# Optimization experiments

Hardware: AMD Instinct MI355X
Metric: run time of the kernel (lower is better)

Reference implementation:

```python
import jax, jax.numpy as jnp
import numpy as np

EMBED_DIM = 768
NUM_HEADS = 8
HEAD_DIM = EMBED_DIM // NUM_HEADS  # 96
SCALE = HEAD_DIM ** -0.5


def setup_inputs() -> dict:
    key = jax.random.key(0)
    k1, k2, k3 = jax.random.split(key, 3)
    x = jax.random.normal(k1, (2, 4096, EMBED_DIM), dtype=jnp.float32)
    # nn.Linear weights stored [out, in]; init scaled like kaiming-uniform-ish
    w_qkv = jax.random.normal(k2, (3 * EMBED_DIM, EMBED_DIM), dtype=jnp.float32) * (EMBED_DIM ** -0.5)
    w_proj = jax.random.normal(k3, (EMBED_DIM, EMBED_DIM), dtype=jnp.float32) * (EMBED_DIM ** -0.5)
    return {"x": x, "w_qkv": w_qkv, "w_proj": w_proj}


def reference(x, w_qkv, w_proj):
    B, N, C = x.shape
    H, D = NUM_HEADS, C // NUM_HEADS
    qkv = jnp.einsum('bnc,oc->bno', x, w_qkv)          # [B,N,3C]
    qkv = qkv.reshape(B, N, 3, H, D).transpose(2, 0, 3, 1, 4)  # [3,B,H,N,D]
    q, k, v = qkv[0], qkv[1], qkv[2]
    attn = jnp.einsum('bhnd,bhmd->bhnm', q, k) * SCALE  # [B,H,N,N]
    attn = jax.nn.softmax(attn, axis=-1)
    out = jnp.einsum('bhnm,bhmd->bhnd', attn, v)        # [B,H,N,D]
    out = out.transpose(0, 2, 1, 3).reshape(B, N, C)
    out = jnp.einsum('bnc,oc->bno', out, w_proj)        # proj (no bias)
    return out  # dropout p=0.0 -> identity
```

## Files before the change

### kernel.cpp

```cpp
#include <hip/hip_runtime.h>

typedef __bf16 bf16;
typedef __attribute__((ext_vector_type(8))) __bf16 bf16x8;
typedef __attribute__((ext_vector_type(2))) __bf16 bf16x2;
typedef __attribute__((ext_vector_type(4))) float f32x4;
typedef __attribute__((ext_vector_type(16))) float f32x16;
typedef __attribute__((ext_vector_type(8))) unsigned short ushort8;
typedef __attribute__((ext_vector_type(4))) unsigned short ushort4v;

__device__ __forceinline__ unsigned short f2bf(float f) {
    union { float f; unsigned int u; } v; v.f = f;
    unsigned int u = v.u;
    return (unsigned short)((u + 0x7fffu + ((u >> 16) & 1u)) >> 16);
}

#if __has_builtin(__builtin_amdgcn_cvt_pk_bf16_f32)
__device__ __forceinline__ unsigned int pk2bf(float a, float b) {
    union { bf16x2 v; unsigned int u; } c;
    c.v = __builtin_amdgcn_cvt_pk_bf16_f32(a, b);
    return c.u;
}
#else
__device__ __forceinline__ unsigned int pk2bf(float a, float b) {
    return (unsigned int)f2bf(a) | ((unsigned int)f2bf(b) << 16);
}
#endif

__device__ __forceinline__ f32x4 mfma16(bf16x8 a, bf16x8 b, f32x4 c) {
    return __builtin_amdgcn_mfma_f32_16x16x32_bf16(a, b, c, 0, 0, 0);
}
__device__ __forceinline__ f32x16 mfma32(bf16x8 a, bf16x8 b, f32x16 c) {
    return __builtin_amdgcn_mfma_f32_32x32x16_bf16(a, b, c, 0, 0, 0);
}

#if __has_builtin(__builtin_amdgcn_global_load_lds)
__device__ __forceinline__ void gload16(const unsigned short* g, unsigned short* l) {
    typedef const unsigned int __attribute__((address_space(1)))* gp_t;
    typedef unsigned int __attribute__((address_space(3)))* lp_t;
    __builtin_amdgcn_global_load_lds((gp_t)(const void*)g, (lp_t)(void*)l, 16, 0, 0);
}
#define GLL_LANE 1
#else
#define GLL_LANE 0
#endif

__global__ void cvt3_f32_bf16(const float* __restrict__ x, const float* __restrict__ wq,
                              const float* __restrict__ wp,
                              unsigned short* __restrict__ xb, unsigned short* __restrict__ wqb,
                              unsigned short* __restrict__ wpb) {
    int i = blockIdx.x * 256 + threadIdx.x;
    const float* in; unsigned short* out; int base;
    if (i < 1572864)      { in = x;  out = xb;  base = i; }
    else if (i < 2015232) { in = wq; out = wqb; base = i - 1572864; }
    else if (i < 2162688) { in = wp; out = wpb; base = i - 2015232; }
    else return;
    float4 f = reinterpret_cast<const float4*>(in)[base];
    union { ushort4v v; unsigned int u[2]; } o;
    o.u[0] = pk2bf(f.x, f.y);
    o.u[1] = pk2bf(f.z, f.w);
    reinterpret_cast<ushort4v*>(out)[base] = o.v;
}

__device__ __forceinline__ int kperm(int k5) {
    return (k5 & 3) | (((k5 >> 3) & 1) << 2) | (((k5 >> 4) & 1) << 3) | (((k5 >> 2) & 1) << 4);
}
__device__ __forceinline__ int kperm_inv(int p5) {
    return (p5 & 3) | (((p5 >> 4) & 1) << 2) | (((p5 >> 2) & 1) << 3) | (((p5 >> 3) & 1) << 4);
}

__global__ __launch_bounds__(256) void qkv_gemm(const unsigned short* __restrict__ A,
                                                const unsigned short* __restrict__ W,
                                                unsigned short* __restrict__ Qf,
                                                unsigned short* __restrict__ Kf,
                                                unsigned short* __restrict__ Vf) {
    __shared__ __align__(16) char smem[34816];
    unsigned short* S = (unsigned short*)smem;
    unsigned short* T = (unsigned short*)smem;
    const int t = threadIdx.x;
    const int w = t >> 6, l = t & 63;
    const int wm = (w >> 1) * 64, wn = (w & 1) * 64;
    const int lr = l & 15, lq = l >> 4;
    const int lqs8 = (lq ^ ((lr >> 1) & 3)) * 8;
    const int m0 = blockIdx.y * 128, n0 = blockIdx.x * 128;
    f32x4 acc[4][4] = {};

#if GLL_LANE
#define QSTAGE(ks, boff)                                                        \
    {                                                                           \
        const int k0s = (ks) * 32;                                              \
        _Pragma("unroll")                                                       \
        for (int i = 0; i < 2; ++i) {                                           \
            int v = t + i * 256;                                                \
            int r = v >> 2, q8 = (((v & 3) ^ ((v >> 3) & 3)) * 8);              \
            unsigned short* dst = &S[(boff) + (w * 64 + i * 256) * 8];          \
            gload16(&A[(m0 + r) * 768 + k0s + q8], dst);                        \
            gload16(&W[(n0 + r) * 768 + k0s + q8], dst + 4096);                 \
        }                                                                       \
    }
#else
#define QSTAGE(ks, boff)                                                        \
    {                                                                           \
        const int k0s = (ks) * 32;                                              \
        _Pragma("unroll")                                                       \
        for (int i = 0; i < 2; ++i) {                                           \
            int v = t + i * 256;                                                \
            int r = v >> 2, q8 = (((v & 3) ^ ((v >> 3) & 3)) * 8);              \
            *reinterpret_cast<ushort8*>(&S[(boff) + v * 8]) =                   \
                *reinterpret_cast<const ushort8*>(&A[(m0 + r) * 768 + k0s + q8]);\
            *reinterpret_cast<ushort8*>(&S[(boff) + 4096 + v * 8]) =            \
                *reinterpret_cast<const ushort8*>(&W[(n0 + r) * 768 + k0s + q8]);\
        }                                                                       \
    }
#endif

    QSTAGE(0, 0);
    __syncthreads();
    for (int ks = 0; ks < 24; ++ks) {
        const int cur = (ks & 1) ? 8192 : 0;
        if (ks < 23) QSTAGE(ks + 1, 8192 - cur);
        bf16x8 af[4], bfr[4];
#pragma unroll
        for (int mt = 0; mt < 4; ++mt)
            af[mt] = *reinterpret_cast<const bf16x8*>(&S[cur + (wm + mt * 16 + lr) * 32 + lqs8]);
#pragma unroll
        for (int nt = 0; nt < 4; ++nt)
            bfr[nt] = *reinterpret_cast<const bf16x8*>(&S[cur + 4096 + (wn + nt * 16 + lr) * 32 + lqs8]);
#pragma unroll
        for (int mt = 0; mt < 4; ++mt)
#pragma unroll
            for (int nt = 0; nt < 4; ++nt)
                acc[mt][nt] = mfma16(af[mt], bfr[nt], acc[mt][nt]);
        __syncthreads();
    }
#undef QSTAGE
    const int tsel = n0 / 768;
    if (tsel < 2) {
#pragma unroll
        for (int nt = 0; nt < 4; ++nt)
#pragma unroll
            for (int mt = 0; mt < 4; ++mt)
#pragma unroll
                for (int r = 0; r < 4; ++r) {
                    int row = wm + mt * 16 + lq * 4 + r;
                    int col = wn + nt * 16 + lr;
                    float val = acc[mt][nt][r];
                    if (tsel == 0) val *= 0.14724444f;
                    T[row * 136 + col] = f2bf(val);
                }
    } else {
#pragma unroll
        for (int nt = 0; nt < 4; ++nt)
#pragma unroll
            for (int mt = 0; mt < 4; ++mt)
#pragma unroll
                for (int r = 0; r < 4; ++r) {
                    int row = wm + mt * 16 + lq * 4 + r;
                    int col = wn + nt * 16 + lr;
                    T[col * 136 + row] = f2bf(acc[mt][nt][r]);
                }
    }
    __syncthreads();
    if (tsel < 2) {
#pragma unroll
        for (int i = 0; i < 8; ++i) {
            int idx = t + i * 256;
            int pos31 = idx & 31;
            int rest = idx >> 5;
            int c8 = rest & 15, qg = rest >> 4;
            int l31 = (tsel == 1) ? kperm_inv(pos31) : pos31;
            int gncol = n0 + c8 * 8;
            int rem = gncol - tsel * 768;
            int head = rem / 96, d = rem - head * 96;
            int kq = d >> 4, h2 = (d >> 3) & 1;
            int gm = m0 + qg * 32 + l31;
            int b = gm >> 12, nn = gm & 4095;
            int bh = b * 8 + head;
            long chunk = (long)(bh * 128 + (nn >> 5)) * 6 + kq;
            ushort8 v8 = *reinterpret_cast<const ushort8*>(&T[(qg * 32 + l31) * 136 + c8 * 8]);
            unsigned short* dst = (tsel == 0) ? Qf : Kf;
            *reinterpret_cast<ushort8*>(&dst[(chunk << 9) + ((h2 * 32 + pos31) << 3)]) = v8;
        }
    } else {
#pragma unroll
        for (int i = 0; i < 8; ++i) {
            int idx = t + i * 256;
            int dl = idx & 31;
            int rr = idx >> 5;
            int r8 = rr & 15, cmb = rr >> 4;
            int col = cmb * 32 + dl;
            int gncol = n0 + col;
            int rem = gncol - 1536;
            int head = rem / 96, d = rem - head * 96;
            int dn = d >> 5;
            int keybase = m0 + r8 * 8;
            int b = keybase >> 12, nn = keybase & 4095;
            int kg = nn >> 5, f = (nn >> 4) & 1, hv = (nn >> 3) & 1;
            int bh = b * 8 + head;
            long chunk = (long)(bh * 128 + kg) * 6 + dn * 2 + f;
            ushort8 v8 = *reinterpret_cast<const ushort8*>(&T[col * 136 + r8 * 8]);
            *reinterpret_cast<ushort8*>(&Vf[(chunk << 9) + ((hv * 32 + dl) << 3)]) = v8;
        }
    }
}

__global__ __launch_bounds__(256, 2) void attn_kernel(const unsigned short* __restrict__ Qf,
                                                      const unsigned short* __restrict__ Kf,
                                                      const unsigned short* __restrict__ Vf,
                                                      unsigned short* __restrict__ Og) {
    __shared__ __align__(16) float red[4608];
    const int t = threadIdx.x;
    const int w = t >> 6, l = t & 63;
    const int wr = w >> 1, wk = w & 1;
    const int l31 = l & 31, h = l >> 5;
    const int b0 = blockIdx.x;
    const int kk = b0 >> 3;
    const int bh = (b0 & 7) * 2 + (kk >> 5);
    const int q0 = (kk & 31) * 128;
    const int voff = l << 3;

    bf16x8 aq[2][6];
#pragma unroll
    for (int qn = 0; qn < 2; ++qn) {
        long qb = ((long)((bh * 128 + (q0 >> 5) + wr * 2 + qn) * 6)) << 9;
#pragma unroll
        for (int kq = 0; kq < 6; ++kq)
            aq[qn][kq] = *reinterpret_cast<const bf16x8*>(&Qf[qb + (kq << 9) + voff]);
    }

    f32x16 acc[2][3] = {};
    float lsum0 = 0.f, lsum1 = 0.f;

    for (int it = 0; it < 64; ++it) {
        const int kt = wk * 64 + it;
        const long kbase = ((long)((bh * 128 + kt) * 6)) << 9;
        f32x16 s[2] = {};
#pragma unroll
        for (int kq = 0; kq < 6; ++kq) {
            bf16x8 bk = *reinterpret_cast<const bf16x8*>(&Kf[kbase + (kq << 9) + voff]);
            s[0] = mfma32(bk, aq[0][kq], s[0]);
            s[1] = mfma32(bk, aq[1][kq], s[1]);
        }
        union PF { unsigned int u[4]; bf16x8 v8; } p[2][2];
#pragma unroll
        for (int qn = 0; qn < 2; ++qn) {
            float e[16];
#pragma unroll
            for (int r = 0; r < 16; ++r) e[r] = __builtin_amdgcn_exp2f(s[qn][r]);
            float s0 = (e[0] + e[1]) + (e[2] + e[3]);
            float s1 = (e[4] + e[5]) + (e[6] + e[7]);
            float s2 = (e[8] + e[9]) + (e[10] + e[11]);
            float s3 = (e[12] + e[13]) + (e[14] + e[15]);
            if (qn == 0) lsum0 += (s0 + s1) + (s2 + s3);
            else         lsum1 += (s0 + s1) + (s2 + s3);
#pragma unroll
            for (int f = 0; f < 2; ++f) {
                p[qn][f].u[0] = pk2bf(e[4 * f + 0], e[4 * f + 1]);
                p[qn][f].u[1] = pk2bf(e[4 * f + 2], e[4 * f + 3]);
                p[qn][f].u[2] = pk2bf(e[8 + 4 * f + 0], e[8 + 4 * f + 1]);
                p[qn][f].u[3] = pk2bf(e[8 + 4 * f + 2], e[8 + 4 * f + 3]);
            }
        }
#pragma unroll
        for (int dn = 0; dn < 3; ++dn) {
#pragma unroll
            for (int f = 0; f < 2; ++f) {
                bf16x8 vb = *reinterpret_cast<const bf16x8*>(
                    &Vf[kbase + ((dn * 2 + f) << 9) + voff]);
                acc[0][dn] = mfma32(p[0][f].v8, vb, acc[0][dn]);
                acc[1][dn] = mfma32(p[1][f].v8, vb, acc[1][dn]);
            }
        }
    }

    const int rbase = (wr * 64 + l) * 36;
#pragma unroll
    for (int ps = 0; ps < 3; ++ps) {
        __syncthreads();
        if (wk == 1) {
#pragma unroll
            for (int c = 0; c < 2; ++c) {
                int c2 = ps * 2 + c, qn = c2 / 3, dn = c2 % 3;
#pragma unroll
                for (int u = 0; u < 4; ++u) {
                    f32x4 tmp;
#pragma unroll
                    for (int j = 0; j < 4; ++j) tmp[j] = acc[qn][dn][u * 4 + j];
                    *reinterpret_cast<f32x4*>(&red[rbase + c * 16 + u * 4]) = tmp;
                }
            }
        }
        __syncthreads();
        if (wk == 0) {
#pragma unroll
            for (int c = 0; c < 2; ++c) {
                int c2 = ps * 2 + c, qn = c2 / 3, dn = c2 % 3;
#pragma unroll
                for (int u = 0; u < 4; ++u) {
                    f32x4 tmp = *reinterpret_cast<const f32x4*>(&red[rbase + c * 16 + u * 4]);
#pragma unroll
                    for (int j = 0; j < 4; ++j) acc[qn][dn][u * 4 + j] += tmp[j];
                }
            }
        }
    }

    lsum0 += __shfl_xor(lsum0, 32);
    lsum1 += __shfl_xor(lsum1, 32);
    __syncthreads();
    if (wk == 1 && h == 0) {
        red[(wr * 2 + 0) * 32 + l31] = lsum0;
        red[(wr * 2 + 1) * 32 + l31] = lsum1;
    }
    __syncthreads();
    if (wk == 0 && h == 0) {
        red[128 + (wr * 2 + 0) * 32 + l31] = 1.f / (lsum0 + red[(wr * 2 + 0) * 32 + l31]);
        red[128 + (wr * 2 + 1) * 32 + l31] = 1.f / (lsum1 + red[(wr * 2 + 1) * 32 + l31]);
    }
    __syncthreads();
    if (wk == 0) {
        const int b = bh >> 3, head = bh & 7;
#pragma unroll
        for (int qn = 0; qn < 2; ++qn) {
#pragma unroll
            for (int reg = 0; reg < 16; ++reg) {
                int qloc = (reg & 3) + 8 * (reg >> 2) + 4 * h;
                int n = q0 + wr * 64 + qn * 32 + qloc;
                float inv = red[128 + (wr * 2 + qn) * 32 + qloc];
                int rowoff = (b * 4096 + n) * 768 + head * 96;
#pragma unroll
                for (int dn = 0; dn < 3; ++dn)
                    Og[rowoff + dn * 32 + l31] = f2bf(acc[qn][dn][reg] * inv);
            }
        }
    }
}

__global__ __launch_bounds__(256) void proj_gemm(const unsigned short* __restrict__ A,
                                                 const unsigned short* __restrict__ W,
                                                 float* __restrict__ out) {
    __shared__ __align__(16) unsigned short S[16384];
    const int t = threadIdx.x;
    const int w = t >> 6, l = t & 63;
    const int wm = (w >> 1) * 64, wn = (w & 1) * 64;
    const int lr = l & 15, lq = l >> 4;
    const int lqs8 = (lq ^ ((lr >> 1) & 3)) * 8;
    const int m0 = blockIdx.y * 128, n0 = blockIdx.x * 128;
    f32x4 acc[4][4] = {};

#if GLL_LANE
#define PSTAGE(ks, boff)                                                        \
    {                                                                           \
        const int k0s = (ks) * 32;                                              \
        _Pragma("unroll")                                                       \
        for (int i = 0; i < 2; ++i) {                                           \
            int v = t + i * 256;                                                \
            int r = v >> 2, q8 = (((v & 3) ^ ((v >> 3) & 3)) * 8);              \
            unsigned short* dst = &S[(boff) + (w * 64 + i * 256) * 8];          \
            gload16(&A[(m0 + r) * 768 + k0s + q8], dst);                        \
            gload16(&W[(n0 + r) * 768 + k0s + q8], dst + 4096);                 \
        }                                                                       \
    }
#else
#define PSTAGE(ks, boff)                                                        \
    {                                                                           \
        const int k0s = (ks) * 32;                                              \
        _Pragma("unroll")                                                       \
        for (int i = 0; i < 2; ++i) {                                           \
            int v = t + i * 256;                                                \
            int r = v >> 2, q8 = (((v & 3) ^ ((v >> 3) & 3)) * 8);              \
            *reinterpret_cast<ushort8*>(&S[(boff) + v * 8]) =                   \
                *reinterpret_cast<const ushort8*>(&A[(m0 + r) * 768 + k0s + q8]);\
            *reinterpret_cast<ushort8*>(&S[(boff) + 4096 + v * 8]) =            \
                *reinterpret_cast<const ushort8*>(&W[(n0 + r) * 768 + k0s + q8]);\
        }                                                                       \
    }
#endif

    PSTAGE(0, 0);
    __syncthreads();
    for (int ks = 0; ks < 24; ++ks) {
        const int cur = (ks & 1) ? 8192 : 0;
        if (ks < 23) PSTAGE(ks + 1, 8192 - cur);
        bf16x8 af[4], bfr[4];
#pragma unroll
        for (int mt = 0; mt < 4; ++mt)
            af[mt] = *reinterpret_cast<const bf16x8*>(&S[cur + (wm + mt * 16 + lr) * 32 + lqs8]);
#pragma unroll
        for (int nt = 0; nt < 4; ++nt)
            bfr[nt] = *reinterpret_cast<const bf16x8*>(&S[cur + 4096 + (wn + nt * 16 + lr) * 32 + lqs8]);
#pragma unroll
        for (int mt = 0; mt < 4; ++mt)
#pragma unroll
            for (int nt = 0; nt < 4; ++nt)
                acc[mt][nt] = mfma16(af[mt], bfr[nt], acc[mt][nt]);
        __syncthreads();
    }
#undef PSTAGE
#pragma unroll
    for (int nt = 0; nt < 4; ++nt) {
        int gn = n0 + wn + nt * 16 + lr;
#pragma unroll
        for (int mt = 0; mt < 4; ++mt) {
#pragma unroll
            for (int r = 0; r < 4; ++r) {
                int gm = m0 + wm + mt * 16 + lq * 4 + r;
                out[gm * 768 + gn] = acc[mt][nt][r];
            }
        }
    }
}

extern "C" void kernel_launch(void* const* d_in, const int* in_sizes, int n_in,
                              void* d_out, int out_size, void* d_ws, size_t ws_size,
                              hipStream_t stream) {
    const float* x     = (const float*)d_in[0];
    const float* wqkv  = (const float*)d_in[1];
    const float* wproj = (const float*)d_in[2];
    float* out = (float*)d_out;
    char* ws = (char*)d_ws;
    unsigned short* xb     = (unsigned short*)(ws);
    unsigned short* wqkvb  = (unsigned short*)(ws + 12582912);
    unsigned short* wprojb = (unsigned short*)(ws + 16121856);
    unsigned short* Qf     = (unsigned short*)(ws + 17301504);
    unsigned short* Kf     = (unsigned short*)(ws + 29884416);
    unsigned short* Vf     = (unsigned short*)(ws + 42467328);
    unsigned short* attnb  = xb;

    cvt3_f32_bf16<<<8448, 256, 0, stream>>>(x, wqkv, wproj, xb, wqkvb, wprojb);
    qkv_gemm<<<dim3(18, 64), 256, 0, stream>>>(xb, wqkvb, Qf, Kf, Vf);
    attn_kernel<<<512, 256, 0, stream>>>(Qf, Kf, Vf, attnb);
    proj_gemm<<<dim3(6, 64), 256, 0, stream>>>(attnb, wprojb, out);
}
```

Measured before the change: 258.1 us.

## Give each wave private LDS tiles in QKV GEMM to drop block barriers

Each wave now stages its own 64-row slices of A and W into a private double-buffered LDS region, so the per-k-step __syncthreads is replaced by per-wave vmcnt waits with a two-stage prefetch. This removes block-wide barrier stalls in the QKV projection GEMM. In exchange, shared memory grows to 64KB per block, which may reduce occupancy. Each wave also loads A and W rows that other waves load too, which duplicates global traffic.

```diff
diff --git a/kernel.cpp b/kernel.cpp
--- a/kernel.cpp
+++ b/kernel.cpp
@@ -73,7 +73,7 @@
                                                 unsigned short* __restrict__ Qf,
                                                 unsigned short* __restrict__ Kf,
                                                 unsigned short* __restrict__ Vf) {
-    __shared__ __align__(16) char smem[34816];
+    __shared__ __align__(16) char smem[65536];
     unsigned short* S = (unsigned short*)smem;
     unsigned short* T = (unsigned short*)smem;
     const int t = threadIdx.x;
@@ -82,57 +82,66 @@
     const int lr = l & 15, lq = l >> 4;
     const int lqs8 = (lq ^ ((lr >> 1) & 3)) * 8;
     const int m0 = blockIdx.y * 128, n0 = blockIdx.x * 128;
+    const int wbase = w * 8192;
     f32x4 acc[4][4] = {};
 
 #if GLL_LANE
-#define QSTAGE(ks, boff)                                                        \
-    {                                                                           \
-        const int k0s = (ks) * 32;                                              \
-        _Pragma("unroll")                                                       \
-        for (int i = 0; i < 2; ++i) {                                           \
-            int v = t + i * 256;                                                \
-            int r = v >> 2, q8 = (((v & 3) ^ ((v >> 3) & 3)) * 8);              \
-            unsigned short* dst = &S[(boff) + (w * 64 + i * 256) * 8];          \
-            gload16(&A[(m0 + r) * 768 + k0s + q8], dst);                        \
-            gload16(&W[(n0 + r) * 768 + k0s + q8], dst + 4096);                 \
-        }                                                                       \
+#define QSTAGE(ks, b)                                                              \
+    {                                                                              \
+        const int k0s = (ks) * 32;                                                 \
+        _Pragma("unroll")                                                          \
+        for (int j = 0; j < 4; ++j) {                                              \
+            int c = j * 64 + l;                                                    \
+            int row = c >> 2, q8 = (((c & 3) ^ ((c >> 3) & 3)) * 8);               \
+            unsigned short* dA = &S[wbase + (b) * 4096 + j * 512];                 \
+            gload16(&A[(m0 + wm + row) * 768 + k0s + q8], dA);                     \
+            gload16(&W[(n0 + wn + row) * 768 + k0s + q8], dA + 2048);              \
+        }                                                                          \
     }
 #else
-#define QSTAGE(ks, boff)                                                        \
-    {                                                                           \
-        const int k0s = (ks) * 32;                                              \
-        _Pragma("unroll")                                                       \
-        for (int i = 0; i < 2; ++i) {                                           \
-            int v = t + i * 256;                                                \
-            int r = v >> 2, q8 = (((v & 3) ^ ((v >> 3) & 3)) * 8);              \
-            *reinterpret_cast<ushort8*>(&S[(boff) + v * 8]) =                   \
-                *reinterpret_cast<const ushort8*>(&A[(m0 + r) * 768 + k0s + q8]);\
-            *reinterpret_cast<ushort8*>(&S[(boff) + 4096 + v * 8]) =            \
-                *reinterpret_cast<const ushort8*>(&W[(n0 + r) * 768 + k0s + q8]);\
-        }                                                                       \
+#define QSTAGE(ks, b)                                                              \
+    {                                                                              \
+        const int k0s = (ks) * 32;                                                 \
+        _Pragma("unroll")                                                          \
+        for (int j = 0; j < 4; ++j) {                                              \
+            int c = j * 64 + l;                                                    \
+            int row = c >> 2, q8 = (((c & 3) ^ ((c >> 3) & 3)) * 8);               \
+            *reinterpret_cast<ushort8*>(&S[wbase + (b) * 4096 + j * 512 + l * 8]) =\
+                *reinterpret_cast<const ushort8*>(&A[(m0 + wm + row) * 768 + k0s + q8]);\
+            *reinterpret_cast<ushort8*>(&S[wbase + (b) * 4096 + 2048 + j * 512 + l * 8]) =\
+                *reinterpret_cast<const ushort8*>(&W[(n0 + wn + row) * 768 + k0s + q8]);\
+        }                                                                          \
     }
 #endif
 
     QSTAGE(0, 0);
-    __syncthreads();
+    asm volatile("s_waitcnt vmcnt(0)" ::: "memory");
+    __builtin_amdgcn_sched_barrier(0);
+    QSTAGE(1, 1);
     for (int ks = 0; ks < 24; ++ks) {
-        const int cur = (ks & 1) ? 8192 : 0;
-        if (ks < 23) QSTAGE(ks + 1, 8192 - cur);
+        if (ks < 23) asm volatile("s_waitcnt vmcnt(8)" ::: "memory");
+        else         asm volatile("s_waitcnt vmcnt(0)" ::: "memory");
+        __builtin_amdgcn_sched_barrier(0);
+        const int cur = ks & 1;
         bf16x8 af[4], bfr[4];
 #pragma unroll
         for (int mt = 0; mt < 4; ++mt)
-            af[mt] = *reinterpret_cast<const bf16x8*>(&S[cur + (wm + mt * 16 + lr) * 32 + lqs8]);
+            af[mt] = *reinterpret_cast<const bf16x8*>(
+                &S[wbase + cur * 4096 + (mt * 16 + lr) * 32 + lqs8]);
 #pragma unroll
         for (int nt = 0; nt < 4; ++nt)
-            bfr[nt] = *reinterpret_cast<const bf16x8*>(&S[cur + 4096 + (wn + nt * 16 + lr) * 32 + lqs8]);
+            bfr[nt] = *reinterpret_cast<const bf16x8*>(
+                &S[wbase + cur * 4096 + 2048 + (nt * 16 + lr) * 32 + lqs8]);
 #pragma unroll
         for (int mt = 0; mt < 4; ++mt)
 #pragma unroll
             for (int nt = 0; nt < 4; ++nt)
                 acc[mt][nt] = mfma16(af[mt], bfr[nt], acc[mt][nt]);
-        __syncthreads();
+        __builtin_amdgcn_sched_barrier(0);
+        if (ks < 22) QSTAGE(ks + 2, cur);
     }
 #undef QSTAGE
+    __syncthreads();
     const int tsel = n0 / 768;
     if (tsel < 2) {
 #pragma unroll
```

Result: slower. 265.8 us (+3.0%).
